# Kernel tuning notes

Hardware: AMD Instinct MI355X
Metric: run time of the kernel (lower is better)

Reference implementation:

```python
import jax, jax.numpy as jnp
import numpy as np

B, T, H, P, F = 65536, 128, 1, 3, 3  # batch, input_length, hidden_dims, pred_var_dims, features


def setup_inputs() -> dict:
    key = jax.random.key(0)
    ks = jax.random.split(key, 8)
    return {
        "history_input": jax.random.normal(ks[0], (B, 1, T, F), dtype=jnp.float32),
        "h0": jnp.zeros((1, B, H), dtype=jnp.float32),
        "c0": jnp.zeros((1, B, H), dtype=jnp.float32),
        "target_acc": jax.random.normal(ks[1], (B, 1, F), dtype=jnp.float32),
        "W_ih": jax.random.normal(ks[2], (4 * H, F), dtype=jnp.float32) * 0.3,
        "W_hh": jax.random.normal(ks[3], (4 * H, H), dtype=jnp.float32) * 0.3,
        "b_ih": jnp.zeros((4 * H,), dtype=jnp.float32),
        "b_hh": jnp.zeros((4 * H,), dtype=jnp.float32),
        "W_mean": jax.random.normal(ks[4], (P, T * H), dtype=jnp.float32) * 0.05,
        "b_mean": jnp.zeros((P,), dtype=jnp.float32),
        "W_var": jax.random.normal(ks[5], (6, T * H), dtype=jnp.float32) * 0.05,
        "b_var": jnp.zeros((6,), dtype=jnp.float32),
    }


def _rotation_matrix(x):
    # x: [B, T, 3]; Gram-Schmidt on last three velocity vectors -> columns of R
    v1, v2, v3 = x[:, -1], x[:, -2], x[:, -3]
    b1 = v1 / jnp.linalg.norm(v1, axis=1, keepdims=True)
    a2 = v2 - jnp.sum(v2 * b1, axis=1, keepdims=True) * b1
    b2 = a2 / jnp.linalg.norm(a2, axis=1, keepdims=True)
    b3 = jnp.cross(b1, b2)
    sign = jnp.where(jnp.sum(v3 * b3, axis=1, keepdims=True) > 0, 1.0, -1.0)
    return jnp.stack([b1, b2, sign * b3], axis=-1)  # [B, 3, 3]


def _lstm(x, h0, c0, W_ih, W_hh, b_ih, b_hh):
    # x: [B, T, F]; PyTorch gate order i, f, g, o
    def step(carry, xt):
        h, c = carry
        g = xt @ W_ih.T + b_ih + h @ W_hh.T + b_hh
        i, f, gg, o = jnp.split(g, 4, axis=-1)
        c = jax.nn.sigmoid(f) * c + jax.nn.sigmoid(i) * jnp.tanh(gg)
        h = jax.nn.sigmoid(o) * jnp.tanh(c)
        return (h, c), h
    (hT, cT), outs = jax.lax.scan(step, (h0, c0), jnp.swapaxes(x, 0, 1))
    return jnp.swapaxes(outs, 0, 1), hT, cT  # [B, T, H]


def reference(history_input, h0, c0, target_acc, W_ih, W_hh, b_ih, b_hh,
              W_mean, b_mean, W_var, b_var):
    x = history_input[:, 0]                      # [B, T, 3]
    R = _rotation_matrix(x)                      # [B, 3, 3]
    rot = jnp.einsum('bji,bkj->bki', R, x)       # R^T @ x_k for each timestep

    out, hT, cT = _lstm(rot, h0[0], c0[0], W_ih, W_hh, b_ih, b_hh)
    feat = out.reshape(out.shape[0], -1)         # [B, T*H]
    means = feat @ W_mean.T + b_mean             # [B, 3]
    elements = feat @ W_var.T + b_var            # [B, 6]

    # unit-lower-triangular L (rows filled per cumsum index = [0, 1, 3])
    eye = jnp.eye(P, dtype=elements.dtype)
    lower = jnp.broadcast_to(eye, (elements.shape[0], P, P))
    lower = lower.at[:, 1, 0].set(elements[:, 0])
    lower = lower.at[:, 2, 0].set(elements[:, 1])
    lower = lower.at[:, 2, 1].set(elements[:, 2])
    dvals = jnp.exp(elements[:, 3:6])            # positive diagonal
    diag = dvals[:, None, :] * eye               # [B, 3, 3]
    sigma = lower @ diag @ jnp.swapaxes(lower, 1, 2)

    rot_target = jnp.einsum('bji,bj->bi', R, target_acc[:, 0])  # R^T @ a
    d = means - rot_target
    sigma_inv = jnp.linalg.inv(sigma)
    quad = jnp.einsum('bi,bij,bj->b', d, sigma_inv, d)
    logprob = -0.5 * dvals.sum(axis=1) - 0.5 * quad
    return -logprob.mean()
```

## Files before the change

kernel.cpp:

```cpp
#include <hip/hip_runtime.h>

#define T_STEPS 128
#define B_TOTAL 65536
#define BLOCK 256
#define NBLOCKS (B_TOTAL / BLOCK)

__device__ __forceinline__ float fast_sigmoid(float x) {
    return 1.0f / (1.0f + __expf(-x));
}
__device__ __forceinline__ float fast_tanh(float x) {
    return 1.0f - 2.0f / (__expf(2.0f * x) + 1.0f);
}

__global__ __launch_bounds__(BLOCK) void lstm_nll_main(
    const float* __restrict__ x,
    const float* __restrict__ h0,
    const float* __restrict__ c0,
    const float* __restrict__ target,
    const float* __restrict__ W_ih,
    const float* __restrict__ W_hh,
    const float* __restrict__ b_ih,
    const float* __restrict__ b_hh,
    const float* __restrict__ W_mean,
    const float* __restrict__ b_mean,
    const float* __restrict__ W_var,
    const float* __restrict__ b_var,
    float* __restrict__ partial)
{
    __shared__ float wpack[T_STEPS * 12];
    __shared__ float wavesum[BLOCK / 64];

    const int tid = threadIdx.x;
    for (int idx = tid; idx < T_STEPS * 12; idx += BLOCK) {
        const int t = idx / 12;
        const int k = idx - t * 12;
        float v = 0.0f;
        if (k < 3)      v = W_mean[k * T_STEPS + t];
        else if (k < 9) v = W_var[(k - 3) * T_STEPS + t];
        wpack[idx] = v;
    }
    __syncthreads();

    const int b = blockIdx.x * BLOCK + tid;
    const float* xb = x + (size_t)b * (T_STEPS * 3);
    const float4* xb4 = (const float4*)xb;

    const float v1x = xb[127*3+0], v1y = xb[127*3+1], v1z = xb[127*3+2];
    const float v2x = xb[126*3+0], v2y = xb[126*3+1], v2z = xb[126*3+2];
    const float v3x = xb[125*3+0], v3y = xb[125*3+1], v3z = xb[125*3+2];

    const float inv1 = rsqrtf(v1x*v1x + v1y*v1y + v1z*v1z);
    const float b1x = v1x*inv1, b1y = v1y*inv1, b1z = v1z*inv1;
    const float dp  = v2x*b1x + v2y*b1y + v2z*b1z;
    const float a2x = v2x - dp*b1x, a2y = v2y - dp*b1y, a2z = v2z - dp*b1z;
    const float inv2 = rsqrtf(a2x*a2x + a2y*a2y + a2z*a2z);
    const float b2x = a2x*inv2, b2y = a2y*inv2, b2z = a2z*inv2;
    float b3x = b1y*b2z - b1z*b2y;
    float b3y = b1z*b2x - b1x*b2z;
    float b3z = b1x*b2y - b1y*b2x;
    const float sgn = (v3x*b3x + v3y*b3y + v3z*b3z) > 0.0f ? 1.0f : -1.0f;
    b3x *= sgn; b3y *= sgn; b3z *= sgn;

    const float wi00 = W_ih[0], wi01 = W_ih[1],  wi02 = W_ih[2];
    const float wi10 = W_ih[3], wi11 = W_ih[4],  wi12 = W_ih[5];
    const float wi20 = W_ih[6], wi21 = W_ih[7],  wi22 = W_ih[8];
    const float wi30 = W_ih[9], wi31 = W_ih[10], wi32 = W_ih[11];
    const float wh0 = W_hh[0], wh1 = W_hh[1], wh2 = W_hh[2], wh3 = W_hh[3];
    const float bg0 = b_ih[0] + b_hh[0];
    const float bg1 = b_ih[1] + b_hh[1];
    const float bg2 = b_ih[2] + b_hh[2];
    const float bg3 = b_ih[3] + b_hh[3];

    float h = h0[b];
    float c = c0[b];
    float m0 = 0.f, m1 = 0.f, m2 = 0.f;
    float e0 = 0.f, e1 = 0.f, e2 = 0.f, e3 = 0.f, e4 = 0.f, e5 = 0.f;

    float4 pre[6];
    #pragma unroll
    for (int q = 0; q < 6; ++q) pre[q] = xb4[q];

    for (int tc = 0; tc < 16; ++tc) {
        float cur[24];
        #pragma unroll
        for (int q = 0; q < 6; ++q) {
            cur[q*4+0] = pre[q].x; cur[q*4+1] = pre[q].y;
            cur[q*4+2] = pre[q].z; cur[q*4+3] = pre[q].w;
        }
        if (tc < 15) {
            #pragma unroll
            for (int q = 0; q < 6; ++q) pre[q] = xb4[(tc + 1) * 6 + q];
        }
        #pragma unroll
        for (int r = 0; r < 8; ++r) {
            const float xx = cur[r*3+0], xy = cur[r*3+1], xz = cur[r*3+2];
            const float r0 = b1x*xx + b1y*xy + b1z*xz;
            const float r1 = b2x*xx + b2y*xy + b2z*xz;
            const float r2 = b3x*xx + b3y*xy + b3z*xz;
            const float gi = wi00*r0 + wi01*r1 + wi02*r2 + wh0*h + bg0;
            const float gf = wi10*r0 + wi11*r1 + wi12*r2 + wh1*h + bg1;
            const float gc = wi20*r0 + wi21*r1 + wi22*r2 + wh2*h + bg2;
            const float go = wi30*r0 + wi31*r1 + wi32*r2 + wh3*h + bg3;
            const float ig = fast_sigmoid(gi);
            const float fg = fast_sigmoid(gf);
            const float tg = fast_tanh(gc);
            const float og = fast_sigmoid(go);
            c = fg * c + ig * tg;
            h = og * fast_tanh(c);
            const int t = tc * 8 + r;
            const float* wp = &wpack[t * 12];
            m0 += wp[0]*h; m1 += wp[1]*h; m2 += wp[2]*h;
            e0 += wp[3]*h; e1 += wp[4]*h; e2 += wp[5]*h;
            e3 += wp[6]*h; e4 += wp[7]*h; e5 += wp[8]*h;
        }
    }

    m0 += b_mean[0]; m1 += b_mean[1]; m2 += b_mean[2];
    e0 += b_var[0]; e1 += b_var[1]; e2 += b_var[2];
    e3 += b_var[3]; e4 += b_var[4]; e5 += b_var[5];

    const float dv0 = __expf(e3), dv1 = __expf(e4), dv2 = __expf(e5);

    const float t0 = target[b*3+0], t1 = target[b*3+1], t2 = target[b*3+2];
    const float rt0 = b1x*t0 + b1y*t1 + b1z*t2;
    const float rt1 = b2x*t0 + b2y*t1 + b2z*t2;
    const float rt2 = b3x*t0 + b3y*t1 + b3z*t2;

    const float d0 = m0 - rt0, d1 = m1 - rt1, d2 = m2 - rt2;
    const float y0 = d0;
    const float y1 = d1 - e0 * y0;
    const float y2 = d2 - e1 * y0 - e2 * y1;
    const float quad = y0*y0/dv0 + y1*y1/dv1 + y2*y2/dv2;

    float contrib = 0.5f * (dv0 + dv1 + dv2) + 0.5f * quad;

    #pragma unroll
    for (int off = 32; off > 0; off >>= 1)
        contrib += __shfl_down(contrib, off, 64);
    const int lane = tid & 63, wid = tid >> 6;
    if (lane == 0) wavesum[wid] = contrib;
    __syncthreads();
    if (tid == 0) {
        float s = 0.f;
        #pragma unroll
        for (int w = 0; w < BLOCK / 64; ++w) s += wavesum[w];
        partial[blockIdx.x] = s;
    }
}

__global__ __launch_bounds__(256) void lstm_nll_finalize(
    const float* __restrict__ partial, float* __restrict__ out, int n)
{
    const int tid = threadIdx.x;
    float s = (tid < n) ? partial[tid] : 0.0f;
    #pragma unroll
    for (int off = 32; off > 0; off >>= 1)
        s += __shfl_down(s, off, 64);
    __shared__ float wavesum[4];
    const int lane = tid & 63, wid = tid >> 6;
    if (lane == 0) wavesum[wid] = s;
    __syncthreads();
    if (tid == 0) {
        out[0] = (wavesum[0] + wavesum[1] + wavesum[2] + wavesum[3]) *
                 (1.0f / (float)B_TOTAL);
    }
}

extern "C" void kernel_launch(void* const* d_in, const int* in_sizes, int n_in,
                              void* d_out, int out_size, void* d_ws, size_t ws_size,
                              hipStream_t stream) {
    const float* x      = (const float*)d_in[0];
    const float* h0     = (const float*)d_in[1];
    const float* c0     = (const float*)d_in[2];
    const float* target = (const float*)d_in[3];
    const float* W_ih   = (const float*)d_in[4];
    const float* W_hh   = (const float*)d_in[5];
    const float* b_ih   = (const float*)d_in[6];
    const float* b_hh   = (const float*)d_in[7];
    const float* W_mean = (const float*)d_in[8];
    const float* b_mean = (const float*)d_in[9];
    const float* W_var  = (const float*)d_in[10];
    const float* b_var  = (const float*)d_in[11];

    float* partial = (float*)d_ws;

    lstm_nll_main<<<NBLOCKS, BLOCK, 0, stream>>>(
        x, h0, c0, target, W_ih, W_hh, b_ih, b_hh,
        W_mean, b_mean, W_var, b_var, partial);
    lstm_nll_finalize<<<1, 256, 0, stream>>>(partial, (float*)d_out, NBLOCKS);
}
```

Measured before the change: 190.5 us.

## Stage input chunks through LDS with coalesced loads and fold rotation into W_ih

```diff
diff --git a/kernel.cpp b/kernel.cpp
--- a/kernel.cpp
+++ b/kernel.cpp
@@ -4,6 +4,11 @@
 #define B_TOTAL 65536
 #define BLOCK 256
 #define NBLOCKS (B_TOTAL / BLOCK)
+#define CH 16
+#define NCH (T_STEPS / CH)
+#define ROWF (CH * 3)
+#define RSTRIDE (ROWF + 1)
+#define FPT 12
 
 __device__ __forceinline__ float fast_sigmoid(float x) {
     return 1.0f / (1.0f + __expf(-x));
@@ -12,7 +17,7 @@
     return 1.0f - 2.0f / (__expf(2.0f * x) + 1.0f);
 }
 
-__global__ __launch_bounds__(BLOCK) void lstm_nll_main(
+__global__ __launch_bounds__(BLOCK, 1) void lstm_nll_main(
     const float* __restrict__ x,
     const float* __restrict__ h0,
     const float* __restrict__ c0,
@@ -27,23 +32,26 @@
     const float* __restrict__ b_var,
     float* __restrict__ partial)
 {
-    __shared__ float wpack[T_STEPS * 12];
-    __shared__ float wavesum[BLOCK / 64];
+    __shared__ float  lds_x[BLOCK * RSTRIDE];
+    __shared__ float4 wpack4[T_STEPS * 3];
+    __shared__ float  wavesum[BLOCK / 64];
 
     const int tid = threadIdx.x;
-    for (int idx = tid; idx < T_STEPS * 12; idx += BLOCK) {
-        const int t = idx / 12;
-        const int k = idx - t * 12;
-        float v = 0.0f;
-        if (k < 3)      v = W_mean[k * T_STEPS + t];
-        else if (k < 9) v = W_var[(k - 3) * T_STEPS + t];
-        wpack[idx] = v;
-    }
-    __syncthreads();
+
+    for (int idx = tid; idx < T_STEPS * 3; idx += BLOCK) {
+        const int t = idx / 3;
+        const int k = idx - t * 3;
+        float4 v;
+        if (k == 0)      v = make_float4(W_mean[0*T_STEPS+t], W_mean[1*T_STEPS+t],
+                                         W_mean[2*T_STEPS+t], W_var[0*T_STEPS+t]);
+        else if (k == 1) v = make_float4(W_var[1*T_STEPS+t], W_var[2*T_STEPS+t],
+                                         W_var[3*T_STEPS+t], W_var[4*T_STEPS+t]);
+        else             v = make_float4(W_var[5*T_STEPS+t], 0.f, 0.f, 0.f);
+        wpack4[idx] = v;
+    }
 
     const int b = blockIdx.x * BLOCK + tid;
     const float* xb = x + (size_t)b * (T_STEPS * 3);
-    const float4* xb4 = (const float4*)xb;
 
     const float v1x = xb[127*3+0], v1y = xb[127*3+1], v1z = xb[127*3+2];
     const float v2x = xb[126*3+0], v2y = xb[126*3+1], v2z = xb[126*3+2];
@@ -65,6 +73,18 @@
     const float wi10 = W_ih[3], wi11 = W_ih[4],  wi12 = W_ih[5];
     const float wi20 = W_ih[6], wi21 = W_ih[7],  wi22 = W_ih[8];
     const float wi30 = W_ih[9], wi31 = W_ih[10], wi32 = W_ih[11];
+    const float wf0x = wi00*b1x + wi01*b2x + wi02*b3x;
+    const float wf0y = wi00*b1y + wi01*b2y + wi02*b3y;
+    const float wf0z = wi00*b1z + wi01*b2z + wi02*b3z;
+    const float wf1x = wi10*b1x + wi11*b2x + wi12*b3x;
+    const float wf1y = wi10*b1y + wi11*b2y + wi12*b3y;
+    const float wf1z = wi10*b1z + wi11*b2z + wi12*b3z;
+    const float wf2x = wi20*b1x + wi21*b2x + wi22*b3x;
+    const float wf2y = wi20*b1y + wi21*b2y + wi22*b3y;
+    const float wf2z = wi20*b1z + wi21*b2z + wi22*b3z;
+    const float wf3x = wi30*b1x + wi31*b2x + wi32*b3x;
+    const float wf3y = wi30*b1y + wi31*b2y + wi32*b3y;
+    const float wf3z = wi30*b1z + wi31*b2z + wi32*b3z;
     const float wh0 = W_hh[0], wh1 = W_hh[1], wh2 = W_hh[2], wh3 = W_hh[3];
     const float bg0 = b_ih[0] + b_hh[0];
     const float bg1 = b_ih[1] + b_hh[1];
@@ -76,42 +96,59 @@
     float m0 = 0.f, m1 = 0.f, m2 = 0.f;
     float e0 = 0.f, e1 = 0.f, e2 = 0.f, e3 = 0.f, e4 = 0.f, e5 = 0.f;
 
-    float4 pre[6];
-    #pragma unroll
-    for (int q = 0; q < 6; ++q) pre[q] = xb4[q];
-
-    for (int tc = 0; tc < 16; ++tc) {
-        float cur[24];
+    const float4* xg4 = (const float4*)(x + (size_t)blockIdx.x * BLOCK * (T_STEPS * 3));
+    int ldsaddr[FPT];
+    int gidx[FPT];
+    #pragma unroll
+    for (int j = 0; j < FPT; ++j) {
+        const int f = j * BLOCK + tid;
+        const int r = f / FPT;
+        const int cc = f - r * FPT;
+        ldsaddr[j] = r * RSTRIDE + cc * 4;
+        gidx[j]    = r * (T_STEPS * 3 / 4) + cc;
+    }
+
+    float4 pre[FPT];
+    #pragma unroll
+    for (int j = 0; j < FPT; ++j) pre[j] = xg4[gidx[j]];
+
+    const float* rowp = &lds_x[tid * RSTRIDE];
+
+    for (int tc = 0; tc < NCH; ++tc) {
+        __syncthreads();
         #pragma unroll
-        for (int q = 0; q < 6; ++q) {
-            cur[q*4+0] = pre[q].x; cur[q*4+1] = pre[q].y;
-            cur[q*4+2] = pre[q].z; cur[q*4+3] = pre[q].w;
+        for (int j = 0; j < FPT; ++j) {
+            lds_x[ldsaddr[j] + 0] = pre[j].x;
+            lds_x[ldsaddr[j] + 1] = pre[j].y;
+            lds_x[ldsaddr[j] + 2] = pre[j].z;
+            lds_x[ldsaddr[j] + 3] = pre[j].w;
         }
-        if (tc < 15) {
+        __syncthreads();
+        if (tc + 1 < NCH) {
+            const int cb = (tc + 1) * FPT;
             #pragma unroll
-            for (int q = 0; q < 6; ++q) pre[q] = xb4[(tc + 1) * 6 + q];
+            for (int j = 0; j < FPT; ++j) pre[j] = xg4[gidx[j] + cb];
         }
         #pragma unroll
-        for (int r = 0; r < 8; ++r) {
-            const float xx = cur[r*3+0], xy = cur[r*3+1], xz = cur[r*3+2];
-            const float r0 = b1x*xx + b1y*xy + b1z*xz;
-            const float r1 = b2x*xx + b2y*xy + b2z*xz;
-            const float r2 = b3x*xx + b3y*xy + b3z*xz;
-            const float gi = wi00*r0 + wi01*r1 + wi02*r2 + wh0*h + bg0;
-            const float gf = wi10*r0 + wi11*r1 + wi12*r2 + wh1*h + bg1;
-            const float gc = wi20*r0 + wi21*r1 + wi22*r2 + wh2*h + bg2;
-            const float go = wi30*r0 + wi31*r1 + wi32*r2 + wh3*h + bg3;
+        for (int s = 0; s < CH; ++s) {
+            const float xx = rowp[s*3+0], xy = rowp[s*3+1], xz = rowp[s*3+2];
+            const float gi = wf0x*xx + wf0y*xy + wf0z*xz + wh0*h + bg0;
+            const float gf = wf1x*xx + wf1y*xy + wf1z*xz + wh1*h + bg1;
+            const float gc = wf2x*xx + wf2y*xy + wf2z*xz + wh2*h + bg2;
+            const float go = wf3x*xx + wf3y*xy + wf3z*xz + wh3*h + bg3;
             const float ig = fast_sigmoid(gi);
             const float fg = fast_sigmoid(gf);
             const float tg = fast_tanh(gc);
             const float og = fast_sigmoid(go);
             c = fg * c + ig * tg;
             h = og * fast_tanh(c);
-            const int t = tc * 8 + r;
-            const float* wp = &wpack[t * 12];
-            m0 += wp[0]*h; m1 += wp[1]*h; m2 += wp[2]*h;
-            e0 += wp[3]*h; e1 += wp[4]*h; e2 += wp[5]*h;
-            e3 += wp[6]*h; e4 += wp[7]*h; e5 += wp[8]*h;
+            const int t = tc * CH + s;
+            const float4 w0 = wpack4[t*3+0];
+            const float4 w1 = wpack4[t*3+1];
+            const float4 w2 = wpack4[t*3+2];
+            m0 += w0.x*h; m1 += w0.y*h; m2 += w0.z*h;
+            e0 += w0.w*h; e1 += w1.x*h; e2 += w1.y*h;
+            e3 += w1.z*h; e4 += w1.w*h; e5 += w2.x*h;
         }
     }
 
```

Result: faster. 183.8 us (-3.5%).
